# Performance work log

Measured on AMD Instinct MI355X. Metric: run time of the kernel, lower is better.

## Reference

```python
import jax, jax.numpy as jnp
import numpy as np

EPS_NORM = 1e-5
EPS_L2 = 1e-12
SCALE_VALUE = 50.0
FROM_VALUE = 0.4
VALUE_INTERVAL = 0.5


def mvn(x):
    # mean-variance norm per (b, c) over spatial dims; torch .var() is unbiased
    mean = jnp.mean(x, axis=(2, 3), keepdims=True)
    var = jnp.var(x, axis=(2, 3), keepdims=True, ddof=1)
    return (x - mean) / jnp.sqrt(var + EPS_NORM)


def conv1x1(x, W, b):
    # x: [b,c,h,w], W: [out,in], b: [out]
    return jnp.einsum('bchw,oc->bohw', x, W) + b[None, :, None, None]


def setup_inputs() -> dict:
    key = jax.random.key(0)
    ks = jax.random.split(key, 12)
    B, C, Hs, Ws = 4, 512, 64, 64
    HW = Hs * Ws  # 4096 == spatial_dims
    HID = HW // 16
    sc = 1.0 / np.sqrt(C)
    inp = {
        'content': jax.random.normal(ks[0], (B, C, Hs, Ws), jnp.float32),
        'style': jax.random.normal(ks[1], (B, C, Hs, Ws), jnp.float32),
        'Wf': jax.random.normal(ks[2], (C, C), jnp.float32) * sc,
        'bf': jnp.zeros((C,), jnp.float32),
        'Wg': jax.random.normal(ks[3], (C, C), jnp.float32) * sc,
        'bg': jnp.zeros((C,), jnp.float32),
        'Wh': jax.random.normal(ks[4], (C, C), jnp.float32) * sc,
        'bh': jnp.zeros((C,), jnp.float32),
        'Wout': jax.random.normal(ks[5], (C, C), jnp.float32) * sc,
        'bout': jnp.zeros((C,), jnp.float32),
        'W1': jax.random.normal(ks[6], (HID, HW), jnp.float32) * (1.0 / np.sqrt(HW)),
        'b1': jnp.zeros((HID,), jnp.float32),
        'W2': jax.random.normal(ks[7], (1, HID), jnp.float32) * (1.0 / np.sqrt(HID)),
        'b2': jnp.zeros((1,), jnp.float32),
    }
    return inp


def reference(content, style, Wf, bf, Wg, bg, Wh, bh, Wout, bout, W1, b1, W2, b2):
    B, C, H, W = content.shape
    HW = H * W

    Fq = conv1x1(mvn(content), Wf, bf).reshape(B, C, HW)   # query feats
    Gk = conv1x1(mvn(style), Wg, bg).reshape(B, C, HW)      # key feats
    Hv = conv1x1(style, Wh, bh).reshape(B, C, HW)           # value feats

    # affinity matrix: channel-L2-normalized cosine similarity [B, HW_c, HW_s]
    cf = content.reshape(B, C, HW)
    sf = style.reshape(B, C, HW)
    cf = cf / jnp.maximum(jnp.linalg.norm(cf, axis=1, keepdims=True), EPS_L2)
    sf = sf / jnp.maximum(jnp.linalg.norm(sf, axis=1, keepdims=True), EPS_L2)
    A = jnp.einsum('bck,bcl->bkl', cf, sf)

    # attention scores + softmax over style positions
    S = jax.nn.softmax(jnp.einsum('bck,bcl->bkl', Fq, Gk), axis=-1)

    # AEAModule: per-content-pixel adaptive clamp from affinity rows
    hmid = jnp.einsum('bkl,ol->bko', A, W1) + b1            # [B, HW, HID]
    hmid = jax.nn.leaky_relu(hmid, 0.2)
    psi = jax.nn.sigmoid(jnp.einsum('bko,po->bkp', hmid, W2) + b2)  # [B, HW, 1]
    clamp_value = psi * VALUE_INTERVAL + FROM_VALUE
    Sg = jax.nn.sigmoid(SCALE_VALUE * (S - clamp_value))    # gated attention

    # O = H @ Sg^T : [B, C, HW_c]
    O = jnp.einsum('bcl,bkl->bck', Hv, Sg).reshape(B, C, H, W)
    O = conv1x1(O, Wout, bout) + content
    return O
```

## Files before the change

### kernel.cpp

```cpp
#include <hip/hip_runtime.h>

typedef unsigned short u16;
typedef __attribute__((ext_vector_type(8))) short short8;
typedef __attribute__((ext_vector_type(4))) float f32x4;

static constexpr int Bn  = 4;
static constexpr int C   = 512;
static constexpr int HW  = 4096;
static constexpr int HID = 256;

__device__ __forceinline__ float bf2f(u16 u){
  union { unsigned int i; float f; } x; x.i = ((unsigned int)u) << 16; return x.f;
}
__device__ __forceinline__ u16 f2bf(float f){
  union { float f; unsigned int i; } x; x.f = f;
  return (u16)((x.i + 0x7fffu + ((x.i >> 16) & 1u)) >> 16);
}
__device__ __forceinline__ float wsum(float v){
  #pragma unroll
  for (int o = 32; o > 0; o >>= 1) v += __shfl_xor(v, o, 64);
  return v;
}
__device__ __forceinline__ float wmax(float v){
  #pragma unroll
  for (int o = 32; o > 0; o >>= 1) v = fmaxf(v, __shfl_xor(v, o, 64));
  return v;
}
__device__ __forceinline__ uint4 pk8(u16 a,u16 b,u16 c,u16 d,u16 e,u16 f,u16 g,u16 h){
  uint4 r; r.x=(unsigned)a|((unsigned)b<<16); r.y=(unsigned)c|((unsigned)d<<16);
  r.z=(unsigned)e|((unsigned)f<<16); r.w=(unsigned)g|((unsigned)h<<16); return r;
}
__device__ __forceinline__ void gld16(const u16* g, u16* l){
  __builtin_amdgcn_global_load_lds((const __attribute__((address_space(1))) void*)g,
                                   (__attribute__((address_space(3))) void*)l, 16, 0, 0);
}

template<bool SPLIT>
__device__ __forceinline__ void mfma_core(const u16* __restrict__ Ah, const u16* __restrict__ Al, int pA,
                                          const u16* __restrict__ Bh, const u16* __restrict__ Bl, int pB,
                                          int K, u16* lds, f32x4 (&acc)[4][4]){
  const int tid  = threadIdx.x;
  const int lane = tid & 63, wave = tid >> 6;
  const int fr = lane & 15, kq = lane >> 4;
  const int kqs = (kq ^ ((fr >> 1) & 3)) * 8;
  const int wm = (wave & 1) * 64, wn = (wave >> 1) * 64;
  constexpr int HB = SPLIT ? 16384 : 8192;
  const int srow = wave*32 + (lane >> 2);
  const int sq   = (((lane & 3) ^ ((lane >> 3) & 3))) * 8;
  const size_t ga = (size_t)srow * pA + sq;
  const size_t gb = (size_t)srow * pB + sq;
  const int ldsc = wave * 1024;

  auto stage = [&](int buf, int k0){
    u16* L = lds + buf*HB;
    #pragma unroll
    for (int i = 0; i < 2; ++i){
      gld16(Ah + ga + (size_t)i*16*pA + k0, L + ldsc + i*512);
      gld16(Bh + gb + (size_t)i*16*pB + k0, L + 4096 + ldsc + i*512);
      if constexpr (SPLIT){
        gld16(Al + ga + (size_t)i*16*pA + k0, L + 8192  + ldsc + i*512);
        gld16(Bl + gb + (size_t)i*16*pB + k0, L + 12288 + ldsc + i*512);
      }
    }
  };
  auto compute = [&](int buf){
    u16* L = lds + buf*HB;
    short8 a[4], b[4];
    #pragma unroll
    for (int i = 0; i < 4; ++i){
      a[i] = *(const short8*)&L[(wm + i*16 + fr)*32 + kqs];
      b[i] = *(const short8*)&L[4096 + (wn + i*16 + fr)*32 + kqs];
    }
    #pragma unroll
    for (int i = 0; i < 4; ++i)
      #pragma unroll
      for (int j = 0; j < 4; ++j)
        acc[i][j] = __builtin_amdgcn_mfma_f32_16x16x32_bf16(a[i], b[j], acc[i][j], 0, 0, 0);
    if constexpr (SPLIT){
      short8 a2[4], b2[4];
      #pragma unroll
      for (int i = 0; i < 4; ++i){
        a2[i] = *(const short8*)&L[8192  + (wm + i*16 + fr)*32 + kqs];
        b2[i] = *(const short8*)&L[12288 + (wn + i*16 + fr)*32 + kqs];
      }
      #pragma unroll
      for (int i = 0; i < 4; ++i)
        #pragma unroll
        for (int j = 0; j < 4; ++j){
          acc[i][j] = __builtin_amdgcn_mfma_f32_16x16x32_bf16(a[i],  b2[j], acc[i][j], 0, 0, 0);
          acc[i][j] = __builtin_amdgcn_mfma_f32_16x16x32_bf16(a2[i], b[j],  acc[i][j], 0, 0, 0);
        }
    }
  };

  stage(0, 0);
  int cur = 0;
  for (int k0 = 32; k0 < K; k0 += 32){
    stage(cur ^ 1, k0);
    if constexpr (SPLIT) asm volatile("s_waitcnt vmcnt(8)" ::: "memory");
    else                 asm volatile("s_waitcnt vmcnt(4)" ::: "memory");
    __builtin_amdgcn_s_barrier();
    compute(cur);
    __builtin_amdgcn_s_barrier();
    cur ^= 1;
  }
  asm volatile("s_waitcnt vmcnt(0)" ::: "memory");
  __builtin_amdgcn_s_barrier();
  compute(cur);
}

struct TileCtx { int wm, wn, cn, rq; };
__device__ __forceinline__ TileCtx tctx(int bx, int by){
  TileCtx t;
  const int wave = threadIdx.x >> 6, lane = threadIdx.x & 63;
  t.wm = by * 128 + (wave & 1) * 64;
  t.wn = bx * 128 + (wave >> 1) * 64;
  t.cn = lane & 15; t.rq = (lane >> 4) * 4;
  return t;
}
#define ACC_ZERO(acc) { _Pragma("unroll") for (int i=0;i<4;++i) _Pragma("unroll") for (int j=0;j<4;++j) _Pragma("unroll") for (int r=0;r<4;++r) acc[i][j][r]=0.f; }

__global__ __launch_bounds__(256) void g_conv_split2(const u16* __restrict__ A0h, const u16* __restrict__ A0l,
                                                     const u16* __restrict__ A1h, const u16* __restrict__ A1l,
                                                     const u16* __restrict__ B0h, const u16* __restrict__ B0l,
                                                     const u16* __restrict__ B1h, const u16* __restrict__ B1l,
                                                     const float* __restrict__ bias0, const float* __restrict__ bias1,
                                                     u16* __restrict__ O0h, u16* __restrict__ O0l,
                                                     u16* __restrict__ O1h, u16* __restrict__ O1l,
                                                     size_t bsA, size_t bsO){
  __shared__ u16 lds[32768];
  const int zb = blockIdx.z, b = zb >> 1, z = zb & 1;
  const u16* Ah = (z ? A1h : A0h) + (size_t)b*bsA;  const u16* Al = (z ? A1l : A0l) + (size_t)b*bsA;
  const u16* Bh = z ? B1h : B0h;  const u16* Bl = z ? B1l : B0l;
  const float* bias = z ? bias1 : bias0;
  u16* Ohi = (z ? O1h : O0h) + (size_t)b*bsO;  u16* Olo = (z ? O1l : O0l) + (size_t)b*bsO;
  TileCtx t = tctx(blockIdx.x, blockIdx.y);
  f32x4 acc[4][4]; ACC_ZERO(acc);
  mfma_core<true>(Ah + (size_t)blockIdx.y*128*C, Al + (size_t)blockIdx.y*128*C, C,
                  Bh + (size_t)blockIdx.x*128*C, Bl + (size_t)blockIdx.x*128*C, C, C, lds, acc);
  #pragma unroll
  for (int fm = 0; fm < 4; ++fm)
    #pragma unroll
    for (int fn = 0; fn < 4; ++fn)
      #pragma unroll
      for (int r = 0; r < 4; ++r){
        int gm = t.wm + fm*16 + t.rq + r;
        int gn = t.wn + fn*16 + t.cn;
        float v = acc[fm][fn][r] + bias[gn];
        u16 h = f2bf(v);
        Ohi[(size_t)gm*C + gn] = h;
        Olo[(size_t)gm*C + gn] = f2bf(v - bf2f(h));
      }
}

__global__ __launch_bounds__(256) void g_gemm_split_f32(const u16* __restrict__ Ah, const u16* __restrict__ Al, int pA,
                                                        const u16* __restrict__ Bh, const u16* __restrict__ Bl, int pB,
                                                        int K, float* __restrict__ O, int pO,
                                                        size_t bsA, size_t bsB, size_t bsO){
  __shared__ u16 lds[32768];
  const int b = blockIdx.z;
  TileCtx t = tctx(blockIdx.x, blockIdx.y);
  f32x4 acc[4][4]; ACC_ZERO(acc);
  mfma_core<true>(Ah + (size_t)b*bsA + (size_t)blockIdx.y*128*pA,
                  Al + (size_t)b*bsA + (size_t)blockIdx.y*128*pA, pA,
                  Bh + (size_t)b*bsB + (size_t)blockIdx.x*128*pB,
                  Bl + (size_t)b*bsB + (size_t)blockIdx.x*128*pB, pB, K, lds, acc);
  float* Ob = O + (size_t)b*bsO;
  #pragma unroll
  for (int fm = 0; fm < 4; ++fm)
    #pragma unroll
    for (int fn = 0; fn < 4; ++fn)
      #pragma unroll
      for (int r = 0; r < 4; ++r)
        Ob[(size_t)(t.wm + fm*16 + t.rq + r)*pO + t.wn + fn*16 + t.cn] = acc[fm][fn][r];
}

__global__ __launch_bounds__(256) void g_gemm_biasm_bf16(const u16* __restrict__ A, int pA,
                                                         const u16* __restrict__ B, int pB,
                                                         int K, const float* __restrict__ bias,
                                                         u16* __restrict__ O, int pO,
                                                         size_t bsB, size_t bsO){
  __shared__ u16 lds[16384];
  const int b = blockIdx.z;
  TileCtx t = tctx(blockIdx.x, blockIdx.y);
  f32x4 acc[4][4]; ACC_ZERO(acc);
  mfma_core<false>(A + (size_t)blockIdx.y*128*pA, nullptr, pA,
                   B + (size_t)b*bsB + (size_t)blockIdx.x*128*pB, nullptr, pB, K, lds, acc);
  u16* Ob = O + (size_t)b*bsO;
  #pragma unroll
  for (int fm = 0; fm < 4; ++fm)
    #pragma unroll
    for (int fn = 0; fn < 4; ++fn)
      #pragma unroll
      for (int r = 0; r < 4; ++r){
        int gm = t.wm + fm*16 + t.rq + r;
        Ob[(size_t)gm*pO + t.wn + fn*16 + t.cn] = f2bf(acc[fm][fn][r] + bias[gm]);
      }
}

__global__ __launch_bounds__(256) void g_gemm_plain_bf16(const u16* __restrict__ A, int pA,
                                                         const u16* __restrict__ B, int pB,
                                                         int K, u16* __restrict__ O, int pO,
                                                         size_t bsA, size_t bsB, size_t bsO){
  __shared__ u16 lds[16384];
  const int b = blockIdx.z;
  TileCtx t = tctx(blockIdx.x, blockIdx.y);
  f32x4 acc[4][4]; ACC_ZERO(acc);
  mfma_core<false>(A + (size_t)b*bsA + (size_t)blockIdx.y*128*pA, nullptr, pA,
                   B + (size_t)b*bsB + (size_t)blockIdx.x*128*pB, nullptr, pB, K, lds, acc);
  u16* Ob = O + (size_t)b*bsO;
  #pragma unroll
  for (int fm = 0; fm < 4; ++fm)
    #pragma unroll
    for (int fn = 0; fn < 4; ++fn)
      #pragma unroll
      for (int r = 0; r < 4; ++r){
        int gm = t.wm + fm*16 + t.rq + r;
        Ob[(size_t)gm*pO + t.wn + fn*16 + t.cn] = f2bf(acc[fm][fn][r]);
      }
}

__global__ __launch_bounds__(256) void g_gemm_partial(const u16* __restrict__ A, int pA,
                                                      const u16* __restrict__ B, int pB,
                                                      int Kper, float* __restrict__ O, int pO,
                                                      size_t sliceStride, int slices,
                                                      size_t bsA, size_t bsB, size_t bsO){
  __shared__ u16 lds[16384];
  const int zz = blockIdx.z;
  const int b = zz / slices, sl = zz - b*slices;
  TileCtx t = tctx(blockIdx.x, blockIdx.y);
  const int koff = sl * Kper;
  f32x4 acc[4][4]; ACC_ZERO(acc);
  mfma_core<false>(A + (size_t)b*bsA + (size_t)blockIdx.y*128*pA + koff, nullptr, pA,
                   B + (size_t)b*bsB + (size_t)blockIdx.x*128*pB + koff, nullptr, pB, Kper, lds, acc);
  float* Oz = O + (size_t)b*bsO + (size_t)sl * sliceStride;
  #pragma unroll
  for (int fm = 0; fm < 4; ++fm)
    #pragma unroll
    for (int fn = 0; fn < 4; ++fn)
      #pragma unroll
      for (int r = 0; r < 4; ++r)
        Oz[(size_t)(t.wm + fm*16 + t.rq + r)*pO + t.wn + fn*16 + t.cn] = acc[fm][fn][r];
}

__global__ __launch_bounds__(256) void k_reduce(const float* __restrict__ in, size_t sliceStride,
                                                int S, u16* __restrict__ out,
                                                size_t bsIn, size_t bsOut){
  const int b = blockIdx.y;
  const float* inb = in + (size_t)b*bsIn;
  u16* outb = out + (size_t)b*bsOut;
  const size_t i4 = ((size_t)blockIdx.x*256 + threadIdx.x) * 4;
  float4 s = *(const float4*)&inb[i4];
  for (int z = 1; z < S; ++z){
    float4 v = *(const float4*)&inb[(size_t)z*sliceStride + i4];
    s.x += v.x; s.y += v.y; s.z += v.z; s.w += v.w;
  }
  u16 r0 = f2bf(s.x), r1 = f2bf(s.y), r2 = f2bf(s.z), r3 = f2bf(s.w);
  uint2 uo; uo.x = (unsigned)r0 | ((unsigned)r1 << 16);
  uo.y = (unsigned)r2 | ((unsigned)r3 << 16);
  *(uint2*)&outb[i4] = uo;
}

__global__ __launch_bounds__(256) void g_gemm_outconv(const u16* __restrict__ A, int pA,
                                                      const u16* __restrict__ B, int pB,
                                                      int K, const float* __restrict__ bias,
                                                      const float* __restrict__ res,
                                                      float* __restrict__ O,
                                                      size_t bsB, size_t bsRes, size_t bsO){
  __shared__ u16 lds[16384];
  const int b = blockIdx.z;
  TileCtx t = tctx(blockIdx.x, blockIdx.y);
  f32x4 acc[4][4]; ACC_ZERO(acc);
  mfma_core<false>(A + (size_t)blockIdx.y*128*pA, nullptr, pA,
                   B + (size_t)b*bsB + (size_t)blockIdx.x*128*pB, nullptr, pB, K, lds, acc);
  const float* resb = res + (size_t)b*bsRes;
  float* Ob = O + (size_t)b*bsO;
  #pragma unroll
  for (int fm = 0; fm < 4; ++fm)
    #pragma unroll
    for (int fn = 0; fn < 4; ++fn)
      #pragma unroll
      for (int r = 0; r < 4; ++r){
        int gm = t.wm + fm*16 + t.rq + r;
        int gn = t.wn + fn*16 + t.cn;
        Ob[(size_t)gm*HW + gn] = acc[fm][fn][r] + bias[gm] + resb[(size_t)gm*HW + gn];
      }
}

__global__ __launch_bounds__(256) void g_gemm_hmid(const u16* __restrict__ A, int pA,
                                                   const u16* __restrict__ B, int pB,
                                                   int K, const float* __restrict__ inc,
                                                   const float* __restrict__ b1,
                                                   float* __restrict__ O,
                                                   size_t bsA, size_t bsP, size_t bsInc, size_t bsO){
  __shared__ u16 lds[16384];
  const int b = blockIdx.z;
  TileCtx t = tctx(blockIdx.x, blockIdx.y);
  f32x4 acc[4][4]; ACC_ZERO(acc);
  mfma_core<false>(A + (size_t)b*bsA + (size_t)blockIdx.y*128*pA, nullptr, pA,
                   B + (size_t)b*bsP + (size_t)blockIdx.x*128*pB, nullptr, pB, K, lds, acc);
  const float* incb = inc + (size_t)b*bsInc;
  float* Ob = O + (size_t)b*bsO;
  #pragma unroll
  for (int fm = 0; fm < 4; ++fm)
    #pragma unroll
    for (int fn = 0; fn < 4; ++fn)
      #pragma unroll
      for (int r = 0; r < 4; ++r){
        int gm = t.wm + fm*16 + t.rq + r;
        int gn = t.wn + fn*16 + t.cn;
        float h = acc[fm][fn][r] * incb[gm] + b1[gn];
        Ob[(size_t)gm*HID + gn] = (h > 0.f) ? h : 0.2f*h;
      }
}

__global__ __launch_bounds__(256) void k_stats(const float* __restrict__ content,
                                               const float* __restrict__ style,
                                               float2* __restrict__ statsC,
                                               float2* __restrict__ statsS){
  const int bc = blockIdx.x;
  const float* X = (blockIdx.y == 0 ? content : style) + (size_t)bc * HW;
  float s = 0.f, sq = 0.f;
  for (int i = threadIdx.x; i < HW; i += 256){ float v = X[i]; s += v; sq += v*v; }
  s = wsum(s); sq = wsum(sq);
  __shared__ float as[4], aq[4];
  if ((threadIdx.x & 63) == 0){ as[threadIdx.x>>6] = s; aq[threadIdx.x>>6] = sq; }
  __syncthreads();
  if (threadIdx.x == 0){
    float S = as[0]+as[1]+as[2]+as[3], Q = aq[0]+aq[1]+aq[2]+aq[3];
    float mean = S / (float)HW;
    float var  = (Q - S*mean) / (float)(HW - 1);
    (blockIdx.y == 0 ? statsC : statsS)[bc] = make_float2(mean, rsqrtf(var + 1e-5f));
  }
}

__global__ __launch_bounds__(256) void k_pixnorm(const float* __restrict__ content,
                                                 const float* __restrict__ style,
                                                 float* __restrict__ inc,
                                                 float* __restrict__ ins){
  const int b = blockIdx.y, z = blockIdx.z;
  const int k0 = blockIdx.x * 64;
  const int kk = threadIdx.x & 63, cg = threadIdx.x >> 6;
  const float* X = (z == 0 ? content : style) + (size_t)b * C * HW + k0 + kk;
  float acc = 0.f;
  for (int c = cg*128; c < cg*128 + 128; ++c){ float v = X[(size_t)c * HW]; acc += v*v; }
  __shared__ float part[4][64];
  part[cg][kk] = acc; __syncthreads();
  if (threadIdx.x < 64){
    float t = part[0][kk] + part[1][kk] + part[2][kk] + part[3][kk];
    (z == 0 ? inc : ins)[b*HW + k0 + kk] = 1.f / fmaxf(sqrtf(t), 1e-12f);
  }
}

__global__ __launch_bounds__(256) void k_prep2(const float* __restrict__ Xc,
                                               const float* __restrict__ Xs,
                                               const float2* __restrict__ stC,
                                               const float2* __restrict__ stSt,
                                               const float* __restrict__ ins,
                                               u16* __restrict__ ThiC, u16* __restrict__ TloC, u16* __restrict__ TrawC,
                                               u16* __restrict__ ThiS, u16* __restrict__ TloS, u16* __restrict__ TrawS,
                                               u16* __restrict__ stSo,
                                               size_t bsX, size_t bsT, int bsSt, size_t bsIns, size_t bsSo){
  const int zb = blockIdx.z, b = zb >> 1, z = zb & 1;
  const float* X = (z ? Xs : Xc) + (size_t)b*bsX;
  const float2* stats = (z ? stSt : stC) + (size_t)b*bsSt;
  u16* Thi = (z ? ThiS : ThiC) + (size_t)b*bsT;
  u16* Tlo = (z ? TloS : TloC) + (size_t)b*bsT;
  u16* Traw = (z ? TrawS : TrawC) + (size_t)b*bsT;
  u16* sSb = stSo + (size_t)b*bsSo;
  const float* insb = ins + (size_t)b*bsIns;
  __shared__ float tile[64][65];
  __shared__ float2 st[64];
  const int k0 = blockIdx.x*64, c0 = blockIdx.y*64;
  const int t = threadIdx.x;
  if (t < 64) st[t] = stats[c0 + t];
  const int j4 = (t & 15) * 4, i0 = t >> 4;
  float4 sv;
  if (z) sv = *(const float4*)&insb[k0 + j4];
  for (int r = 0; r < 4; ++r){
    int i = i0 + r*16;
    float4 v = *(const float4*)&X[(size_t)(c0+i)*HW + k0 + j4];
    tile[i][j4+0] = v.x; tile[i][j4+1] = v.y; tile[i][j4+2] = v.z; tile[i][j4+3] = v.w;
    if (z){
      u16 q0 = f2bf(v.x*sv.x), q1 = f2bf(v.y*sv.y), q2 = f2bf(v.z*sv.z), q3 = f2bf(v.w*sv.w);
      uint2 uo; uo.x = (unsigned)q0 | ((unsigned)q1 << 16);
      uo.y = (unsigned)q2 | ((unsigned)q3 << 16);
      *(uint2*)&sSb[(size_t)(c0+i)*HW + k0 + j4] = uo;
    }
  }
  __syncthreads();
  const int kk = t >> 2, cc = (t & 3) * 16;
  u16 h[16], l[16], rw[16];
  #pragma unroll
  for (int q = 0; q < 16; ++q){
    float x = tile[cc+q][kk];
    float2 s = st[cc+q];
    rw[q] = f2bf(x);
    float v = (x - s.x) * s.y;
    h[q] = f2bf(v);
    l[q] = f2bf(v - bf2f(h[q]));
  }
  size_t o = (size_t)(k0+kk)*C + c0 + cc;
  *(uint4*)&Thi[o]    = pk8(h[0],h[1],h[2],h[3],h[4],h[5],h[6],h[7]);
  *(uint4*)&Thi[o+8]  = pk8(h[8],h[9],h[10],h[11],h[12],h[13],h[14],h[15]);
  *(uint4*)&Tlo[o]    = pk8(l[0],l[1],l[2],l[3],l[4],l[5],l[6],l[7]);
  *(uint4*)&Tlo[o+8]  = pk8(l[8],l[9],l[10],l[11],l[12],l[13],l[14],l[15]);
  *(uint4*)&Traw[o]   = pk8(rw[0],rw[1],rw[2],rw[3],rw[4],rw[5],rw[6],rw[7]);
  *(uint4*)&Traw[o+8] = pk8(rw[8],rw[9],rw[10],rw[11],rw[12],rw[13],rw[14],rw[15]);
}

__global__ __launch_bounds__(256) void k_wprep(const float* __restrict__ Wf, const float* __restrict__ Wg,
                                               const float* __restrict__ Wh, const float* __restrict__ Wo,
                                               const float* __restrict__ W1,
                                               u16* __restrict__ Wfh, u16* __restrict__ Wfl,
                                               u16* __restrict__ Wgh, u16* __restrict__ Wgl,
                                               u16* __restrict__ Whb, u16* __restrict__ Wob,
                                               u16* __restrict__ W1b){
  const int idx = (blockIdx.x*256 + threadIdx.x) * 4;
  const int mode = blockIdx.y;
  const int nsmall = C*C;
  if (mode == 4){
    float4 v = *(const float4*)&W1[idx];
    W1b[idx+0]=f2bf(v.x); W1b[idx+1]=f2bf(v.y); W1b[idx+2]=f2bf(v.z); W1b[idx+3]=f2bf(v.w);
    return;
  }
  if (idx >= nsmall) return;
  const float* src = (mode==0)?Wf:(mode==1)?Wg:(mode==2)?Wh:Wo;
  float4 v = *(const float4*)&src[idx];
  float vv[4] = {v.x, v.y, v.z, v.w};
  if (mode <= 1){
    u16* oh = (mode==0)?Wfh:Wgh;  u16* ol = (mode==0)?Wfl:Wgl;
    #pragma unroll
    for (int q = 0; q < 4; ++q){
      u16 hh = f2bf(vv[q]);
      oh[idx+q] = hh; ol[idx+q] = f2bf(vv[q] - bf2f(hh));
    }
  } else {
    u16* ob = (mode==2)?Whb:Wob;
    #pragma unroll
    for (int q = 0; q < 4; ++q) ob[idx+q] = f2bf(vv[q]);
  }
}

__global__ __launch_bounds__(256) void k_psi(const float* __restrict__ hmid,
                                             const float* __restrict__ W2,
                                             const float* __restrict__ b2,
                                             float* __restrict__ clampv,
                                             size_t bsH, size_t bsC){
  const int k = blockIdx.x, tid = threadIdx.x, b = blockIdx.y;
  float v = hmid[(size_t)b*bsH + (size_t)k*HID + tid] * W2[tid];
  v = wsum(v);
  __shared__ float a[4];
  if ((tid & 63) == 0) a[tid>>6] = v;
  __syncthreads();
  if (tid == 0){
    float t = a[0]+a[1]+a[2]+a[3];
    float psi = 1.f/(1.f + __expf(-(t + b2[0])));
    clampv[(size_t)b*bsC + k] = psi*0.5f + 0.4f;
  }
}

__global__ __launch_bounds__(256) void k_softgate(float* __restrict__ T2,
                                                  const float* __restrict__ clampv,
                                                  size_t bsT, size_t bsC){
  const int k = blockIdx.x, tid = threadIdx.x, b = blockIdx.y;
  float* row = &T2[(size_t)b*bsT + (size_t)k*HW];
  float vals[16];
  float mx = -3.4e38f;
  #pragma unroll
  for (int i = 0; i < 16; ++i){ vals[i] = row[tid + i*256]; mx = fmaxf(mx, vals[i]); }
  mx = wmax(mx);
  __shared__ float am[4], asm_[4];
  if ((tid & 63) == 0) am[tid>>6] = mx;
  __syncthreads();
  mx = fmaxf(fmaxf(am[0], am[1]), fmaxf(am[2], am[3]));
  float s = 0.f;
  #pragma unroll
  for (int i = 0; i < 16; ++i){ vals[i] = __expf(vals[i] - mx); s += vals[i]; }
  s = wsum(s);
  if ((tid & 63) == 0) asm_[tid>>6] = s;
  __syncthreads();
  s = asm_[0]+asm_[1]+asm_[2]+asm_[3];
  const float inv = 1.f / s;
  const float cv = clampv[(size_t)b*bsC + k];
  u16* Sg = (u16*)row;
  #pragma unroll
  for (int i = 0; i < 16; ++i){
    float sg = 1.f/(1.f + __expf(-50.f*(vals[i]*inv - cv)));
    Sg[tid + i*256] = f2bf(sg);
  }
}

extern "C" void kernel_launch(void* const* d_in, const int* in_sizes, int n_in,
                              void* d_out, int out_size, void* d_ws, size_t ws_size,
                              hipStream_t stream){
  const float* content = (const float*)d_in[0];
  const float* style   = (const float*)d_in[1];
  const float* Wf   = (const float*)d_in[2];  const float* bfv  = (const float*)d_in[3];
  const float* Wg   = (const float*)d_in[4];  const float* bg   = (const float*)d_in[5];
  const float* Wh   = (const float*)d_in[6];  const float* bh   = (const float*)d_in[7];
  const float* Wo   = (const float*)d_in[8];  const float* bout = (const float*)d_in[9];
  const float* W1   = (const float*)d_in[10]; const float* b1   = (const float*)d_in[11];
  const float* W2   = (const float*)d_in[12]; const float* b2   = (const float*)d_in[13];
  float* out = (float*)d_out;
  (void)in_sizes; (void)n_in; (void)out_size;

  char* ws = (char*)d_ws;
  size_t off = 0;
  auto alloc = [&](size_t bytes)->void*{
    void* p = (void*)(ws + off);
    off += (bytes + 255) & ~(size_t)255;
    return p;
  };
  float2* statsC = (float2*)alloc((size_t)Bn*C*sizeof(float2));
  float2* statsS = (float2*)alloc((size_t)Bn*C*sizeof(float2));
  float*  inc    = (float*) alloc((size_t)Bn*HW*sizeof(float));
  float*  ins    = (float*) alloc((size_t)Bn*HW*sizeof(float));
  float*  clampv = (float*) alloc((size_t)Bn*HW*sizeof(float));
  u16* Wfh = (u16*)alloc((size_t)C*C*2), *Wfl = (u16*)alloc((size_t)C*C*2);
  u16* Wgh = (u16*)alloc((size_t)C*C*2), *Wgl = (u16*)alloc((size_t)C*C*2);
  u16* Whb = (u16*)alloc((size_t)C*C*2), *Wob = (u16*)alloc((size_t)C*C*2);
  u16* W1b = (u16*)alloc((size_t)HID*HW*2);
  const size_t commonEnd = off;

  const size_t TPB = (size_t)HW*C;
  const size_t XB  = (size_t)C*HW;
  const size_t SLB = (size_t)Bn*TPB*2;

  k_stats  <<<dim3(Bn*C, 2),       256, 0, stream>>>(content, style, statsC, statsS);
  k_pixnorm<<<dim3(HW/64, Bn, 2),  256, 0, stream>>>(content, style, inc, ins);
  k_wprep  <<<dim3(HID*HW/1024, 5),256, 0, stream>>>(Wf, Wg, Wh, Wo, W1,
                                                     Wfh, Wfl, Wgh, Wgl, Whb, Wob, W1b);

  auto runPrep = [&](char* R, u16* bFqTh, u16* bFqTl, u16* bGkTh, u16* bGkTl,
                     u16* bHvb, u16* bPT){
    u16* bXcTh = (u16*)(R + 0*SLB);
    u16* bXcTl = (u16*)(R + 1*SLB);
    u16* bXsTh = (u16*)(R + 2*SLB);
    u16* bXsTl = (u16*)(R + 3*SLB);
    u16* bCrT  = (u16*)(R + 4*SLB);
    u16* bSrT  = (u16*)(R + 5*SLB);
    u16* bstS  = (u16*)(R + 6*SLB);
    float* bPpart = (float*)(R + 0*SLB);
    float* bhmid  = (float*)(R + 1*SLB);
    k_prep2 <<<dim3(HW/64, C/64, 2*Bn), 256, 0, stream>>>(content, style, statsC, statsS, ins,
                                                          bXcTh, bXcTl, bCrT, bXsTh, bXsTl, bSrT,
                                                          bstS, XB, TPB, C, HW, TPB);
    g_conv_split2<<<dim3(C/128, HW/128, 2*Bn), 256, 0, stream>>>(
        bXcTh, bXcTl, bXsTh, bXsTl, Wfh, Wfl, Wgh, Wgl, bfv, bg,
        bFqTh, bFqTl, bGkTh, bGkTl, TPB, TPB);
    g_gemm_biasm_bf16<<<dim3(HW/128, C/128, Bn), 256, 0, stream>>>(Whb, C, bSrT, C, C, bh,
                                                                   bHvb, HW, TPB, TPB);
    g_gemm_partial<<<dim3(C/128, HID/128, Bn*16), 256, 0, stream>>>(W1b, HW, bstS, HW, 256,
                                                                    bPpart, C, (size_t)HID*C, 16,
                                                                    0, TPB, (size_t)16*HID*C);
    k_reduce<<<dim3(HID*C/1024, Bn), 256, 0, stream>>>(bPpart, (size_t)HID*C, 16, bPT,
                                                       (size_t)16*HID*C, (size_t)HID*C);
    g_gemm_hmid<<<dim3(HID/128, HW/128, Bn), 256, 0, stream>>>(bCrT, C, bPT, C, C, inc, b1, bhmid,
                                                               TPB, (size_t)HID*C, HW, (size_t)HW*HID);
    k_psi<<<dim3(HW, Bn), 256, 0, stream>>>(bhmid, W2, b2, clampv, (size_t)HW*HID, HW);
  };

  {
    size_t o = commonEnd;
    auto al = [&](size_t bytes)->void*{ void* p = (void*)(ws + o); o += (bytes + 255) & ~(size_t)255; return p; };
    u16* bFqTh = (u16*)al(SLB), *bFqTl = (u16*)al(SLB);
    u16* bGkTh = (u16*)al(SLB), *bGkTl = (u16*)al(SLB);
    u16* bHvb  = (u16*)al(SLB);
    u16* bPT   = (u16*)al((size_t)Bn*HID*C*2);
    u16* bO1T  = (u16*)al(SLB);
    char* R    = (char*)al((size_t)Bn*HW*HW*4);
    if (o <= ws_size){
      runPrep(R, bFqTh, bFqTl, bGkTh, bGkTl, bHvb, bPT);
      float* bT2 = (float*)R;
      g_gemm_split_f32<<<dim3(HW/128, HW/128, Bn), 256, 0, stream>>>(bFqTh, bFqTl, C, bGkTh, bGkTl, C,
                                                                     C, bT2, HW,
                                                                     TPB, TPB, (size_t)HW*HW);
      k_softgate<<<dim3(HW, Bn), 256, 0, stream>>>(bT2, clampv, (size_t)HW*HW, HW);
      g_gemm_plain_bf16<<<dim3(C/128, HW/128, Bn), 256, 0, stream>>>((const u16*)bT2, 2*HW, bHvb, HW,
                                                                     HW, bO1T, C,
                                                                     (size_t)HW*HW*2, TPB, TPB);
      g_gemm_outconv<<<dim3(HW/128, C/128, Bn), 256, 0, stream>>>(Wob, C, bO1T, C, C, bout, content, out,
                                                                  TPB, XB, XB);
      return;
    }
  }

  {
    size_t o = commonEnd;
    auto al = [&](size_t bytes)->void*{ void* p = (void*)(ws + o); o += (bytes + 255) & ~(size_t)255; return p; };
    u16* bFqTh = (u16*)al(SLB), *bFqTl = (u16*)al(SLB);
    u16* bGkTh = (u16*)al(SLB), *bGkTl = (u16*)al(SLB);
    u16* bHvb  = (u16*)al(SLB);
    u16* bPT   = (u16*)al((size_t)Bn*HID*C*2);
    char* R    = (char*)al((size_t)2*HW*HW*4 + (size_t)4*HW*C*4 + (size_t)2*TPB*2);
    if (o <= ws_size){
      runPrep(R, bFqTh, bFqTl, bGkTh, bGkTl, bHvb, bPT);
      float* T2s   = (float*)R;
      float* Opart = (float*)(R + (size_t)2*HW*HW*4);
      u16*   O1Ts  = (u16*)(R + (size_t)2*HW*HW*4 + (size_t)4*HW*C*4);
      for (int cb = 0; cb < Bn; cb += 2){
        g_gemm_split_f32<<<dim3(HW/128, HW/128, 2), 256, 0, stream>>>(
            bFqTh + (size_t)cb*TPB, bFqTl + (size_t)cb*TPB, C,
            bGkTh + (size_t)cb*TPB, bGkTl + (size_t)cb*TPB, C, C, T2s, HW,
            TPB, TPB, (size_t)HW*HW);
        k_softgate<<<dim3(HW, 2), 256, 0, stream>>>(T2s, clampv + (size_t)cb*HW,
                                                    (size_t)HW*HW, HW);
        g_gemm_partial<<<dim3(C/128, HW/128, 4), 256, 0, stream>>>(
            (const u16*)T2s, 2*HW, bHvb + (size_t)cb*TPB, HW, 2048,
            Opart, C, (size_t)HW*C, 2,
            (size_t)HW*HW*2, TPB, (size_t)2*HW*C);
        k_reduce<<<dim3(HW*C/1024, 2), 256, 0, stream>>>(Opart, (size_t)HW*C, 2, O1Ts,
                                                         (size_t)2*HW*C, TPB);
        g_gemm_outconv<<<dim3(HW/128, C/128, 2), 256, 0, stream>>>(
            Wob, C, O1Ts, C, C, bout, content + (size_t)cb*XB, out + (size_t)cb*XB,
            TPB, XB, XB);
      }
      return;
    }
  }

  {
    size_t o = commonEnd;
    auto al = [&](size_t bytes)->void*{ void* p = (void*)(ws + o); o += (bytes + 255) & ~(size_t)255; return p; };
    u16* bFqTh = (u16*)al(SLB), *bFqTl = (u16*)al(SLB);
    u16* bGkTh = (u16*)al(SLB), *bGkTl = (u16*)al(SLB);
    u16* bHvb  = (u16*)al(SLB);
    u16* bPT   = (u16*)al((size_t)Bn*HID*C*2);
    char* R    = (char*)al((size_t)2*HW*HW*4 + (size_t)2*TPB*2 + 256);
    if (o <= ws_size){
      runPrep(R, bFqTh, bFqTl, bGkTh, bGkTl, bHvb, bPT);
      float* T2s  = (float*)R;
      u16*   O1Ts = (u16*)(R + (size_t)2*HW*HW*4);
      for (int cb = 0; cb < Bn; cb += 2){
        g_gemm_split_f32<<<dim3(HW/128, HW/128, 2), 256, 0, stream>>>(
            bFqTh + (size_t)cb*TPB, bFqTl + (size_t)cb*TPB, C,
            bGkTh + (size_t)cb*TPB, bGkTl + (size_t)cb*TPB, C, C, T2s, HW,
            TPB, TPB, (size_t)HW*HW);
        k_softgate<<<dim3(HW, 2), 256, 0, stream>>>(T2s, clampv + (size_t)cb*HW,
                                                    (size_t)HW*HW, HW);
        g_gemm_plain_bf16<<<dim3(C/128, HW/128, 2), 256, 0, stream>>>(
            (const u16*)T2s, 2*HW, bHvb + (size_t)cb*TPB, HW, HW, O1Ts, C,
            (size_t)HW*HW*2, TPB, TPB);
        g_gemm_outconv<<<dim3(HW/128, C/128, 2), 256, 0, stream>>>(
            Wob, C, O1Ts, C, C, bout, content + (size_t)cb*XB, out + (size_t)cb*XB,
            TPB, XB, XB);
      }
      return;
    }
  }

  {
    size_t o = commonEnd;
    auto al = [&](size_t bytes)->void*{ void* p = (void*)(ws + o); o += (bytes + 255) & ~(size_t)255; return p; };
    u16* bFqTh = (u16*)al(SLB), *bFqTl = (u16*)al(SLB);
    u16* bGkTh = (u16*)al(SLB), *bGkTl = (u16*)al(SLB);
    u16* bHvb  = (u16*)al(SLB);
    u16* bPT   = (u16*)al((size_t)Bn*HID*C*2);
    char* R    = (char*)al(7*SLB);
    if (o <= ws_size){
      runPrep(R, bFqTh, bFqTl, bGkTh, bGkTl, bHvb, bPT);
      float* T2s   = (float*)(R + 0*SLB);
      float* Opart = (float*)(R + 4*SLB);
      u16*   O1Ts  = (u16*)  (R + 6*SLB);
      for (int b = 0; b < Bn; ++b){
        g_gemm_split_f32<<<dim3(HW/128, HW/128), 256, 0, stream>>>(
            bFqTh + (size_t)b*TPB, bFqTl + (size_t)b*TPB, C,
            bGkTh + (size_t)b*TPB, bGkTl + (size_t)b*TPB, C, C, T2s, HW, 0, 0, 0);
        k_softgate<<<dim3(HW), 256, 0, stream>>>(T2s, clampv + (size_t)b*HW, 0, 0);
        g_gemm_partial<<<dim3(C/128, HW/128, 4), 256, 0, stream>>>(
            (const u16*)T2s, 2*HW, bHvb + (size_t)b*TPB, HW, 1024,
            Opart, C, (size_t)HW*C, 4, 0, 0, 0);
        k_reduce<<<dim3(HW*C/1024), 256, 0, stream>>>(Opart, (size_t)HW*C, 4, O1Ts, 0, 0);
        g_gemm_outconv<<<dim3(HW/128, C/128), 256, 0, stream>>>(Wob, C, O1Ts, C, C, bout,
            content + (size_t)b*XB, out + (size_t)b*XB, 0, 0, 0);
      }
      return;
    }
  }

  off = commonEnd;
  u16* XcTh = (u16*)alloc((size_t)HW*C*2), *XcTl = (u16*)alloc((size_t)HW*C*2);
  u16* CrT  = (u16*)alloc((size_t)HW*C*2);
  u16* XsTh = (u16*)alloc((size_t)HW*C*2), *XsTl = (u16*)alloc((size_t)HW*C*2);
  u16* SrT  = (u16*)alloc((size_t)HW*C*2);
  u16* stS  = (u16*)alloc((size_t)C*HW*2);
  u16* FqTh = (u16*)alloc((size_t)HW*C*2), *FqTl = (u16*)alloc((size_t)HW*C*2);
  u16* GkTh = (u16*)alloc((size_t)HW*C*2), *GkTl = (u16*)alloc((size_t)HW*C*2);
  u16* Hvb  = (u16*)alloc((size_t)C*HW*2);
  u16* O1T  = (u16*)alloc((size_t)HW*C*2);
  u16* PT   = (u16*)alloc((size_t)HID*C*2);
  float* hmid  = (float*)alloc((size_t)HW*HID*sizeof(float));
  float* Ppart = (float*)alloc((size_t)16*HID*C*sizeof(float));
  float* Opart = (float*)alloc((size_t)4*HW*C*sizeof(float));
  float* T2    = (float*)alloc((size_t)HW*HW*sizeof(float));

  for (int b = 0; b < Bn; ++b){
    const float* cb = content + (size_t)b*C*HW;
    const float* sb = style   + (size_t)b*C*HW;
    const float* incb = inc + (size_t)b*HW;
    const float* insb = ins + (size_t)b*HW;
    float* clb = clampv + (size_t)b*HW;

    k_prep2 <<<dim3(HW/64, C/64, 2), 256, 0, stream>>>(cb, sb, statsC + (size_t)b*C, statsS + (size_t)b*C,
                                                       insb, XcTh, XcTl, CrT, XsTh, XsTl, SrT,
                                                       stS, 0, 0, 0, 0, 0);
    g_conv_split2<<<dim3(C/128, HW/128, 2), 256, 0, stream>>>(
        XcTh, XcTl, XsTh, XsTl, Wfh, Wfl, Wgh, Wgl, bfv, bg,
        FqTh, FqTl, GkTh, GkTl, 0, 0);
    g_gemm_biasm_bf16<<<dim3(HW/128, C/128), 256, 0, stream>>>(Whb, C, SrT, C, C, bh, Hvb, HW, 0, 0);
    g_gemm_partial<<<dim3(C/128, HID/128, 16), 256, 0, stream>>>(W1b, HW, stS, HW, 256,
                                                                 Ppart, C, (size_t)HID*C, 16, 0, 0, 0);
    k_reduce<<<dim3(HID*C/1024), 256, 0, stream>>>(Ppart, (size_t)HID*C, 16, PT, 0, 0);
    g_gemm_hmid<<<dim3(HID/128, HW/128), 256, 0, stream>>>(CrT, C, PT, C, C, incb, b1, hmid, 0, 0, 0, 0);
    k_psi<<<dim3(HW), 256, 0, stream>>>(hmid, W2, b2, clb, 0, 0);
    g_gemm_split_f32<<<dim3(HW/128, HW/128), 256, 0, stream>>>(FqTh, FqTl, C, GkTh, GkTl, C, C, T2, HW, 0, 0, 0);
    k_softgate<<<dim3(HW), 256, 0, stream>>>(T2, clb, 0, 0);
    g_gemm_partial<<<dim3(C/128, HW/128, 4), 256, 0, stream>>>((const u16*)T2, 2*HW, Hvb, HW, 1024,
                                                               Opart, C, (size_t)HW*C, 4, 0, 0, 0);
    k_reduce<<<dim3(HW*C/1024), 256, 0, stream>>>(Opart, (size_t)HW*C, 4, O1T, 0, 0);
    g_gemm_outconv<<<dim3(HW/128, C/128), 256, 0, stream>>>(Wob, C, O1T, C, C, bout, cb,
                                                            out + (size_t)b*C*HW, 0, 0, 0);
  }
}
```

Before: 744.2 us.

## Triple-buffer non-split GEMM mainloop and split-K attention-value GEMM into softgate buffer

The non-split MFMA mainloop moves from double to triple LDS buffering, keeping two stages of global loads in flight to hide memory latency better. In exchange each block uses more LDS, which may reduce how many blocks fit per CU. The attention-times-value GEMM now splits K in two. Its fp32 partials are written into the unused upper half of each softgate row (bf16 data occupies only the first half), so the separate partial buffer and one code path are dropped. A new two-way reduce kernel reads both partials from those rows and converts them to bf16.

```diff
diff --git a/kernel.cpp b/kernel.cpp
--- a/kernel.cpp
+++ b/kernel.cpp
@@ -93,20 +93,40 @@
     }
   };
 
-  stage(0, 0);
-  int cur = 0;
-  for (int k0 = 32; k0 < K; k0 += 32){
-    stage(cur ^ 1, k0);
-    if constexpr (SPLIT) asm volatile("s_waitcnt vmcnt(8)" ::: "memory");
-    else                 asm volatile("s_waitcnt vmcnt(4)" ::: "memory");
+  if constexpr (SPLIT){
+    stage(0, 0);
+    int cur = 0;
+    for (int k0 = 32; k0 < K; k0 += 32){
+      stage(cur ^ 1, k0);
+      asm volatile("s_waitcnt vmcnt(8)" ::: "memory");
+      __builtin_amdgcn_s_barrier();
+      compute(cur);
+      __builtin_amdgcn_s_barrier();
+      cur ^= 1;
+    }
+    asm volatile("s_waitcnt vmcnt(0)" ::: "memory");
+    __builtin_amdgcn_s_barrier();
+    compute(cur);
+  } else {
+    stage(0, 0); stage(1, 32);
+    int cur = 0;
+    for (int k0 = 64; k0 < K; k0 += 32){
+      stage(cur == 0 ? 2 : cur - 1, k0);
+      asm volatile("s_waitcnt vmcnt(8)" ::: "memory");
+      __builtin_amdgcn_s_barrier();
+      compute(cur);
+      __builtin_amdgcn_s_barrier();
+      cur = (cur == 2) ? 0 : cur + 1;
+    }
+    asm volatile("s_waitcnt vmcnt(4)" ::: "memory");
     __builtin_amdgcn_s_barrier();
     compute(cur);
     __builtin_amdgcn_s_barrier();
-    cur ^= 1;
-  }
-  asm volatile("s_waitcnt vmcnt(0)" ::: "memory");
-  __builtin_amdgcn_s_barrier();
-  compute(cur);
+    cur = (cur == 2) ? 0 : cur + 1;
+    asm volatile("s_waitcnt vmcnt(0)" ::: "memory");
+    __builtin_amdgcn_s_barrier();
+    compute(cur);
+  }
 }
 
 struct TileCtx { int wm, wn, cn, rq; };
@@ -180,7 +200,7 @@
                                                          int K, const float* __restrict__ bias,
                                                          u16* __restrict__ O, int pO,
                                                          size_t bsB, size_t bsO){
-  __shared__ u16 lds[16384];
+  __shared__ u16 lds[24576];
   const int b = blockIdx.z;
   TileCtx t = tctx(blockIdx.x, blockIdx.y);
   f32x4 acc[4][4]; ACC_ZERO(acc);
@@ -202,7 +222,7 @@
                                                          const u16* __restrict__ B, int pB,
                                                          int K, u16* __restrict__ O, int pO,
                                                          size_t bsA, size_t bsB, size_t bsO){
-  __shared__ u16 lds[16384];
+  __shared__ u16 lds[24576];
   const int b = blockIdx.z;
   TileCtx t = tctx(blockIdx.x, blockIdx.y);
   f32x4 acc[4][4]; ACC_ZERO(acc);
@@ -225,7 +245,7 @@
                                                       int Kper, float* __restrict__ O, int pO,
                                                       size_t sliceStride, int slices,
                                                       size_t bsA, size_t bsB, size_t bsO){
-  __shared__ u16 lds[16384];
+  __shared__ u16 lds[24576];
   const int zz = blockIdx.z;
   const int b = zz / slices, sl = zz - b*slices;
   TileCtx t = tctx(blockIdx.x, blockIdx.y);
@@ -261,13 +281,29 @@
   *(uint2*)&outb[i4] = uo;
 }
 
+__global__ __launch_bounds__(256) void k_reduce2(const float* __restrict__ in, size_t bsIn,
+                                                 u16* __restrict__ out, size_t bsOut){
+  const int b = blockIdx.y;
+  const float* inb = in + (size_t)b*bsIn;
+  u16* outb = out + (size_t)b*bsOut;
+  const size_t i4 = ((size_t)blockIdx.x*256 + threadIdx.x) * 4;
+  const int k = (int)(i4 >> 9), c = (int)(i4 & 511);
+  const float* row = inb + (size_t)k*HW;
+  float4 a = *(const float4*)&row[c];
+  float4 q = *(const float4*)&row[512 + c];
+  uint2 uo;
+  uo.x = (unsigned)f2bf(a.x+q.x) | ((unsigned)f2bf(a.y+q.y) << 16);
+  uo.y = (unsigned)f2bf(a.z+q.z) | ((unsigned)f2bf(a.w+q.w) << 16);
+  *(uint2*)&outb[i4] = uo;
+}
+
 __global__ __launch_bounds__(256) void g_gemm_outconv(const u16* __restrict__ A, int pA,
                                                       const u16* __restrict__ B, int pB,
                                                       int K, const float* __restrict__ bias,
                                                       const float* __restrict__ res,
                                                       float* __restrict__ O,
                                                       size_t bsB, size_t bsRes, size_t bsO){
-  __shared__ u16 lds[16384];
+  __shared__ u16 lds[24576];
   const int b = blockIdx.z;
   TileCtx t = tctx(blockIdx.x, blockIdx.y);
   f32x4 acc[4][4]; ACC_ZERO(acc);
@@ -293,7 +329,7 @@
                                                    const float* __restrict__ b1,
                                                    float* __restrict__ O,
                                                    size_t bsA, size_t bsP, size_t bsInc, size_t bsO){
-  __shared__ u16 lds[16384];
+  __shared__ u16 lds[24576];
   const int b = blockIdx.z;
   TileCtx t = tctx(blockIdx.x, blockIdx.y);
   f32x4 acc[4][4]; ACC_ZERO(acc);
@@ -577,45 +613,14 @@
                                                                      C, bT2, HW,
                                                                      TPB, TPB, (size_t)HW*HW);
       k_softgate<<<dim3(HW, Bn), 256, 0, stream>>>(bT2, clampv, (size_t)HW*HW, HW);
-      g_gemm_plain_bf16<<<dim3(C/128, HW/128, Bn), 256, 0, stream>>>((const u16*)bT2, 2*HW, bHvb, HW,
-                                                                     HW, bO1T, C,
-                                                                     (size_t)HW*HW*2, TPB, TPB);
+      g_gemm_partial<<<dim3(C/128, HW/128, Bn*2), 256, 0, stream>>>(
+          (const u16*)bT2, 2*HW, bHvb, HW, 2048,
+          (float*)bT2 + 2048, HW, 512, 2,
+          (size_t)HW*HW*2, TPB, (size_t)HW*HW);
+      k_reduce2<<<dim3(HW*C/1024, Bn), 256, 0, stream>>>((float*)bT2 + 2048, (size_t)HW*HW,
+                                                         bO1T, TPB);
       g_gemm_outconv<<<dim3(HW/128, C/128, Bn), 256, 0, stream>>>(Wob, C, bO1T, C, C, bout, content, out,
                                                                   TPB, XB, XB);
-      return;
-    }
-  }
-
-  {
-    size_t o = commonEnd;
-    auto al = [&](size_t bytes)->void*{ void* p = (void*)(ws + o); o += (bytes + 255) & ~(size_t)255; return p; };
-    u16* bFqTh = (u16*)al(SLB), *bFqTl = (u16*)al(SLB);
-    u16* bGkTh = (u16*)al(SLB), *bGkTl = (u16*)al(SLB);
-    u16* bHvb  = (u16*)al(SLB);
-    u16* bPT   = (u16*)al((size_t)Bn*HID*C*2);
-    char* R    = (char*)al((size_t)2*HW*HW*4 + (size_t)4*HW*C*4 + (size_t)2*TPB*2);
-    if (o <= ws_size){
-      runPrep(R, bFqTh, bFqTl, bGkTh, bGkTl, bHvb, bPT);
-      float* T2s   = (float*)R;
-      float* Opart = (float*)(R + (size_t)2*HW*HW*4);
-      u16*   O1Ts  = (u16*)(R + (size_t)2*HW*HW*4 + (size_t)4*HW*C*4);
-      for (int cb = 0; cb < Bn; cb += 2){
-        g_gemm_split_f32<<<dim3(HW/128, HW/128, 2), 256, 0, stream>>>(
-            bFqTh + (size_t)cb*TPB, bFqTl + (size_t)cb*TPB, C,
-            bGkTh + (size_t)cb*TPB, bGkTl + (size_t)cb*TPB, C, C, T2s, HW,
-            TPB, TPB, (size_t)HW*HW);
-        k_softgate<<<dim3(HW, 2), 256, 0, stream>>>(T2s, clampv + (size_t)cb*HW,
-                                                    (size_t)HW*HW, HW);
-        g_gemm_partial<<<dim3(C/128, HW/128, 4), 256, 0, stream>>>(
-            (const u16*)T2s, 2*HW, bHvb + (size_t)cb*TPB, HW, 2048,
-            Opart, C, (size_t)HW*C, 2,
-            (size_t)HW*HW*2, TPB, (size_t)2*HW*C);
-        k_reduce<<<dim3(HW*C/1024, 2), 256, 0, stream>>>(Opart, (size_t)HW*C, 2, O1Ts,
-                                                         (size_t)2*HW*C, TPB);
-        g_gemm_outconv<<<dim3(HW/128, C/128, 2), 256, 0, stream>>>(
-            Wob, C, O1Ts, C, C, bout, content + (size_t)cb*XB, out + (size_t)cb*XB,
-            TPB, XB, XB);
-      }
       return;
     }
   }
@@ -639,9 +644,12 @@
             TPB, TPB, (size_t)HW*HW);
         k_softgate<<<dim3(HW, 2), 256, 0, stream>>>(T2s, clampv + (size_t)cb*HW,
                                                     (size_t)HW*HW, HW);
-        g_gemm_plain_bf16<<<dim3(C/128, HW/128, 2), 256, 0, stream>>>(
-            (const u16*)T2s, 2*HW, bHvb + (size_t)cb*TPB, HW, HW, O1Ts, C,
-            (size_t)HW*HW*2, TPB, TPB);
+        g_gemm_partial<<<dim3(C/128, HW/128, 4), 256, 0, stream>>>(
+            (const u16*)T2s, 2*HW, bHvb + (size_t)cb*TPB, HW, 2048,
+            T2s + 2048, HW, 512, 2,
+            (size_t)HW*HW*2, TPB, (size_t)HW*HW);
+        k_reduce2<<<dim3(HW*C/1024, 2), 256, 0, stream>>>(T2s + 2048, (size_t)HW*HW,
+                                                          O1Ts, TPB);
         g_gemm_outconv<<<dim3(HW/128, C/128, 2), 256, 0, stream>>>(
             Wob, C, O1Ts, C, C, bout, content + (size_t)cb*XB, out + (size_t)cb*XB,
             TPB, XB, XB);
@@ -661,17 +669,17 @@
     if (o <= ws_size){
       runPrep(R, bFqTh, bFqTl, bGkTh, bGkTl, bHvb, bPT);
       float* T2s   = (float*)(R + 0*SLB);
-      float* Opart = (float*)(R + 4*SLB);
       u16*   O1Ts  = (u16*)  (R + 6*SLB);
       for (int b = 0; b < Bn; ++b){
         g_gemm_split_f32<<<dim3(HW/128, HW/128), 256, 0, stream>>>(
             bFqTh + (size_t)b*TPB, bFqTl + (size_t)b*TPB, C,
             bGkTh + (size_t)b*TPB, bGkTl + (size_t)b*TPB, C, C, T2s, HW, 0, 0, 0);
         k_softgate<<<dim3(HW), 256, 0, stream>>>(T2s, clampv + (size_t)b*HW, 0, 0);
-        g_gemm_partial<<<dim3(C/128, HW/128, 4), 256, 0, stream>>>(
-            (const u16*)T2s, 2*HW, bHvb + (size_t)b*TPB, HW, 1024,
-            Opart, C, (size_t)HW*C, 4, 0, 0, 0);
-        k_reduce<<<dim3(HW*C/1024), 256, 0, stream>>>(Opart, (size_t)HW*C, 4, O1Ts, 0, 0);
+        g_gemm_partial<<<dim3(C/128, HW/128, 2), 256, 0, stream>>>(
+            (const u16*)T2s, 2*HW, bHvb + (size_t)b*TPB, HW, 2048,
+            T2s + 2048, HW, 512, 2,
+            0, 0, 0);
+        k_reduce2<<<dim3(HW*C/1024), 256, 0, stream>>>(T2s + 2048, 0, O1Ts, 0);
         g_gemm_outconv<<<dim3(HW/128, C/128), 256, 0, stream>>>(Wob, C, O1Ts, C, C, bout,
             content + (size_t)b*XB, out + (size_t)b*XB, 0, 0, 0);
       }
@@ -692,7 +700,6 @@
   u16* PT   = (u16*)alloc((size_t)HID*C*2);
   float* hmid  = (float*)alloc((size_t)HW*HID*sizeof(float));
   float* Ppart = (float*)alloc((size_t)16*HID*C*sizeof(float));
-  float* Opart = (float*)alloc((size_t)4*HW*C*sizeof(float));
   float* T2    = (float*)alloc((size_t)HW*HW*sizeof(float));
 
   for (int b = 0; b < Bn; ++b){
@@ -716,9 +723,9 @@
     k_psi<<<dim3(HW), 256, 0, stream>>>(hmid, W2, b2, clb, 0, 0);
     g_gemm_split_f32<<<dim3(HW/128, HW/128), 256, 0, stream>>>(FqTh, FqTl, C, GkTh, GkTl, C, C, T2, HW, 0, 0, 0);
     k_softgate<<<dim3(HW), 256, 0, stream>>>(T2, clb, 0, 0);
-    g_gemm_partial<<<dim3(C/128, HW/128, 4), 256, 0, stream>>>((const u16*)T2, 2*HW, Hvb, HW, 1024,
-                                                               Opart, C, (size_t)HW*C, 4, 0, 0, 0);
-    k_reduce<<<dim3(HW*C/1024), 256, 0, stream>>>(Opart, (size_t)HW*C, 4, O1T, 0, 0);
+    g_gemm_partial<<<dim3(C/128, HW/128, 2), 256, 0, stream>>>(
+        (const u16*)T2, 2*HW, Hvb, HW, 2048, T2 + 2048, HW, 512, 2, 0, 0, 0);
+    k_reduce2<<<dim3(HW*C/1024), 256, 0, stream>>>(T2 + 2048, 0, O1T, 0);
     g_gemm_outconv<<<dim3(HW/128, C/128), 256, 0, stream>>>(Wob, C, O1T, C, C, bout, cb,
                                                             out + (size_t)b*C*HW, 0, 0, 0);
   }
```

Result: slower. 778.4 us (+4.6%).
